# Kernel optimization log

Hardware: AMD Instinct MI355X
Metric: run time of the kernel (lower is better)

The kernel has to match this reference:

```python
import jax, jax.numpy as jnp
import numpy as np

T, B, I, H = 4096, 2048, 1, 10


def setup_inputs() -> dict:
    key = jax.random.key(0)
    ks = jax.random.split(key, 8)
    k = 1.0 / np.sqrt(H)  # torch default init bound for RNN and Linear(10,1)
    u = lambda kk, shape: jax.random.uniform(kk, shape, jnp.float32, -k, k)
    return {
        "x": jax.random.normal(ks[0], (T, B, I), jnp.float32),
        "h": jnp.zeros((1, B, H), jnp.float32),
        "W_ih": u(ks[1], (H, I)),
        "b_ih": u(ks[2], (H,)),
        "W_hh": u(ks[3], (H, H)),
        "b_hh": u(ks[4], (H,)),
        "W_out": u(ks[5], (1, H)),
        "b_out": u(ks[6], (1,)),
    }


def reference(x, h, W_ih, b_ih, W_hh, b_hh, W_out, b_out):
    # Vanilla RNN: h_t = tanh(x_t @ W_ih^T + b_ih + h_{t-1} @ W_hh^T + b_hh)
    b = b_ih + b_hh  # fuse the two biases once

    def step(h_prev, x_t):  # h_prev: [B,H], x_t: [B,I]
        h_new = jnp.tanh(x_t @ W_ih.T + h_prev @ W_hh.T + b)
        return h_new, h_new

    h_last, ys = jax.lax.scan(step, h[0], x)  # ys: [T,B,H]
    out = ys @ W_out.T + b_out  # [T,B,1]
    return out, h_last[None]  # h: [1,B,H]
```

## Files before the change

### kernel.cpp

```cpp
#include <hip/hip_runtime.h>

#define T_STEPS 4096
#define BATCH   2048
#define HID     10
#define UB      16

__device__ __forceinline__ void issue16(float (&xr)[UB], const float* base) {
#pragma unroll
    for (int u = 0; u < UB; ++u)
        asm volatile("global_load_dword %0, %1, off"
                     : "=v"(xr[u]) : "v"(base + (size_t)u * BATCH) : "memory");
}
#define BIND16(a) "+v"(a[0]),"+v"(a[1]),"+v"(a[2]),"+v"(a[3]),"+v"(a[4]), \
    "+v"(a[5]),"+v"(a[6]),"+v"(a[7]),"+v"(a[8]),"+v"(a[9]),"+v"(a[10]),   \
    "+v"(a[11]),"+v"(a[12]),"+v"(a[13]),"+v"(a[14]),"+v"(a[15])
__device__ __forceinline__ void wait1_bind(float (&xr)[UB]) {
    asm volatile("s_waitcnt vmcnt(1)" : BIND16(xr) :: "memory");
}
__device__ __forceinline__ void wait0_bind(float (&xr)[UB]) {
    asm volatile("s_waitcnt vmcnt(0)" : BIND16(xr) :: "memory");
}

#define STEP_HEAD \
    "v_fma_f32 %[c0], %[wih2], %[x], %[bj2]\n\t"                                    \
    "v_fmac_f32 %[c0], %[r], %[w0]\n\t"                                             \
    "v_mul_f32_dpp %[c1], %[r], %[w1] row_ror:1 row_mask:0xf bank_mask:0xf\n\t"     \
    "v_fmac_f32_dpp %[c0], %[r], %[w2] row_ror:2 row_mask:0xf bank_mask:0xf\n\t"    \
    "v_fmac_f32_dpp %[c1], %[r], %[w3] row_ror:3 row_mask:0xf bank_mask:0xf\n\t"    \
    "v_fmac_f32_dpp %[c0], %[r], %[w4] row_ror:4 row_mask:0xf bank_mask:0xf\n\t"    \
    "v_fmac_f32_dpp %[c1], %[r], %[w5] row_ror:5 row_mask:0xf bank_mask:0xf\n\t"    \
    "v_fmac_f32_dpp %[c0], %[r], %[w6] row_ror:6 row_mask:0xf bank_mask:0xf\n\t"    \
    "v_fmac_f32_dpp %[c1], %[r], %[w7] row_ror:7 row_mask:0xf bank_mask:0xf\n\t"    \
    "v_fmac_f32_dpp %[c0], %[r], %[w8] row_ror:8 row_mask:0xf bank_mask:0xf\n\t"    \
    "v_fmac_f32_dpp %[c1], %[r], %[w9] row_ror:9 row_mask:0xf bank_mask:0xf\n\t"    \
    "v_fmac_f32_dpp %[c0], %[r], %[w10] row_ror:10 row_mask:0xf bank_mask:0xf\n\t"  \
    "v_fmac_f32_dpp %[c1], %[r], %[w11] row_ror:11 row_mask:0xf bank_mask:0xf\n\t"  \
    "v_fmac_f32_dpp %[c0], %[r], %[w12] row_ror:12 row_mask:0xf bank_mask:0xf\n\t"  \
    "v_fmac_f32_dpp %[c1], %[r], %[w13] row_ror:13 row_mask:0xf bank_mask:0xf\n\t"  \
    "v_fmac_f32_dpp %[c0], %[r], %[w14] row_ror:14 row_mask:0xf bank_mask:0xf\n\t"  \
    "v_fmac_f32_dpp %[c1], %[r], %[w15] row_ror:15 row_mask:0xf bank_mask:0xf\n\t"  \
    "v_add_f32 %[c0], %[c0], %[c1]\n\t"                                             \
    "v_exp_f32 %[ex], %[c0]\n\t"                                                    \
    "s_nop 0\n\t"                                                                   \
    "v_add_f32 %[ex], 1.0, %[ex]\n\t"

#define STEP_TAIL \
    "v_rcp_f32 %[r], %[ex]\n\t"                                                     \
    "s_nop 0"

#define PKDPP(N) "v_fmac_f32_dpp %[pk], %[c0], %[m] row_ror:" #N " row_mask:0xf bank_mask:0xf\n\t"
#define PKPLAIN  "v_fmac_f32 %[pk], %[c0], %[m]\n\t"

#define DEF_STEP(SUF, PKLINE_) \
__device__ __forceinline__ void step_##SUF(float& r, float& pk, float x, \
        float wih2, float bj2, float m, const float (&w)[16]) { \
    float c0, c1, ex; \
    asm volatile( STEP_HEAD PKLINE_ STEP_TAIL \
        : [c0]"=&v"(c0), [c1]"=&v"(c1), [ex]"=&v"(ex), \
          [r]"+v"(r), [pk]"+v"(pk) \
        : [x]"v"(x), [wih2]"v"(wih2), [bj2]"v"(bj2), [m]"v"(m), \
          [w0]"v"(w[0]),  [w1]"v"(w[1]),  [w2]"v"(w[2]),  [w3]"v"(w[3]), \
          [w4]"v"(w[4]),  [w5]"v"(w[5]),  [w6]"v"(w[6]),  [w7]"v"(w[7]), \
          [w8]"v"(w[8]),  [w9]"v"(w[9]),  [w10]"v"(w[10]),[w11]"v"(w[11]), \
          [w12]"v"(w[12]),[w13]"v"(w[13]),[w14]"v"(w[14]),[w15]"v"(w[15])); \
}

DEF_STEP(r0,  PKPLAIN)
DEF_STEP(r1,  PKDPP(1))
DEF_STEP(r2,  PKDPP(2))
DEF_STEP(r3,  PKDPP(3))
DEF_STEP(r4,  PKDPP(4))
DEF_STEP(r5,  PKDPP(5))
DEF_STEP(r6,  PKDPP(6))
DEF_STEP(r7,  PKDPP(7))
DEF_STEP(r8,  PKDPP(8))
DEF_STEP(r9,  PKDPP(9))
DEF_STEP(r10, PKDPP(10))
DEF_STEP(r11, PKDPP(11))
DEF_STEP(r12, PKDPP(12))
DEF_STEP(r13, PKDPP(13))
DEF_STEP(r14, PKDPP(14))
DEF_STEP(r15, PKDPP(15))

template<int U>
__device__ __forceinline__ void step_u(float& r, float& pk, float x,
                                       float wih2, float bj2,
                                       const float (&km)[16],
                                       const float (&w)[16]) {
    constexpr int ROT = (U + 5) & 15;
    const float m = km[(U + 15) & 15];
    if constexpr (ROT == 0)       step_r0 (r, pk, x, wih2, bj2, m, w);
    else if constexpr (ROT == 1)  step_r1 (r, pk, x, wih2, bj2, m, w);
    else if constexpr (ROT == 2)  step_r2 (r, pk, x, wih2, bj2, m, w);
    else if constexpr (ROT == 3)  step_r3 (r, pk, x, wih2, bj2, m, w);
    else if constexpr (ROT == 4)  step_r4 (r, pk, x, wih2, bj2, m, w);
    else if constexpr (ROT == 5)  step_r5 (r, pk, x, wih2, bj2, m, w);
    else if constexpr (ROT == 6)  step_r6 (r, pk, x, wih2, bj2, m, w);
    else if constexpr (ROT == 7)  step_r7 (r, pk, x, wih2, bj2, m, w);
    else if constexpr (ROT == 8)  step_r8 (r, pk, x, wih2, bj2, m, w);
    else if constexpr (ROT == 9)  step_r9 (r, pk, x, wih2, bj2, m, w);
    else if constexpr (ROT == 10) step_r10(r, pk, x, wih2, bj2, m, w);
    else if constexpr (ROT == 11) step_r11(r, pk, x, wih2, bj2, m, w);
    else if constexpr (ROT == 12) step_r12(r, pk, x, wih2, bj2, m, w);
    else if constexpr (ROT == 13) step_r13(r, pk, x, wih2, bj2, m, w);
    else if constexpr (ROT == 14) step_r14(r, pk, x, wih2, bj2, m, w);
    else                          step_r15(r, pk, x, wih2, bj2, m, w);
}

template<int U>
__device__ __forceinline__ void run16(float& r, float& pk, const float (&xr)[UB],
                                      float wih2, float bj2,
                                      const float (&km)[16],
                                      const float (&w)[16]) {
    if constexpr (U < UB) {
        step_u<U>(r, pk, xr[U], wih2, bj2, km, w);
        run16<U + 1>(r, pk, xr, wih2, bj2, km, w);
    }
}

__device__ __forceinline__ void finish_reduce(float r, float& p, float& pk,
                                              float wo2, float m0) {
    asm volatile(
        "v_mul_f32 %[p], %[wo2], %[r]\n\t"
        "s_nop 1\n\t"
        "v_add_f32_dpp %[p], %[p], %[p] row_ror:8 row_mask:0xf bank_mask:0xf\n\t"
        "s_nop 1\n\t"
        "v_add_f32_dpp %[p], %[p], %[p] row_ror:4 row_mask:0xf bank_mask:0xf\n\t"
        "s_nop 1\n\t"
        "v_add_f32_dpp %[p], %[p], %[p] row_ror:2 row_mask:0xf bank_mask:0xf\n\t"
        "s_nop 1\n\t"
        "v_add_f32_dpp %[p], %[p], %[p] row_ror:1 row_mask:0xf bank_mask:0xf\n\t"
        "s_nop 1\n\t"
        "v_fmac_f32 %[pk], %[p], %[m]"
        : [p]"+v"(p), [pk]"+v"(pk)
        : [r]"v"(r), [wo2]"v"(wo2), [m]"v"(m0));
}

__global__ __launch_bounds__(64, 1) void rnn_kernel(
    const float* __restrict__ x,
    const float* __restrict__ h0,
    const float* __restrict__ W_ih,
    const float* __restrict__ b_ih,
    const float* __restrict__ W_hh,
    const float* __restrict__ b_hh,
    const float* __restrict__ W_out,
    const float* __restrict__ b_out,
    float* __restrict__ out)
{
    const int tid = threadIdx.x;
    const int j   = tid & 15;
    const int b   = (blockIdx.x << 2) + (tid >> 4);
    const bool jv = (j < HID);
    const int jc  = jv ? j : 0;

    const float CC = 2.88539008177792681472f;

    const float wih = jv ? W_ih[jc] : 0.0f;
    const float bj  = jv ? (b_ih[jc] + b_hh[jc]) : 0.0f;
    const float wo  = jv ? W_out[jc] : 0.0f;

    float wsh[16];
    float wsum = 0.0f;
#pragma unroll
    for (int N = 0; N < 16; ++N) {
        const int k = (j - N) & 15;
        wsh[N] = (jv && k < HID) ? W_hh[jc * HID + k] : 0.0f;
        wsum += wsh[N];
    }

    const float wih2 = CC * wih;
    const float bj2  = CC * (bj + wsum);
    float w2[16];
#pragma unroll
    for (int N = 0; N < 16; ++N) {
        if (jv) {
            w2[N] = -2.0f * CC * wsh[N];
        } else if (j == 10) {
            const int k = (10 - N) & 15;
            w2[N] = (k < HID) ? (-2.0f * W_out[k]) : 0.0f;
        } else {
            w2[N] = 0.0f;
        }
    }
    const float wo2 = -2.0f * wo;
    float c0sum = b_out[0];
#pragma unroll
    for (int k = 0; k < HID; ++k) c0sum += W_out[k];

    float km[16];
#pragma unroll
    for (int i = 0; i < 16; ++i) km[i] = (j == i) ? 1.0f : 0.0f;

    float rval = fmaf(-0.5f, jv ? h0[b * HID + jc] : 0.0f, 0.5f);
    float pk = 0.0f;

    const float* xb = x + b;
    float xA[UB], xB[UB];

    issue16(xA, xb);
    wait0_bind(xA);

    for (int t0 = 0; t0 < T_STEPS; t0 += 2 * UB) {
        wait1_bind(xA);
        issue16(xB, xb + (size_t)(t0 + UB) * BATCH);
        run16<0>(rval, pk, xA, wih2, bj2, km, w2);
        {
            const int tj = t0 + ((j == 15) ? -1 : j);
            if (tj >= 0) out[(size_t)tj * BATCH + b] = pk + c0sum;
        }
        pk = 0.0f;

        wait1_bind(xB);
        const float* xsrc = (t0 + 2 * UB < T_STEPS)
                          ? (xb + (size_t)(t0 + 2 * UB) * BATCH) : xb;
        issue16(xA, xsrc);
        run16<0>(rval, pk, xB, wih2, bj2, km, w2);
        {
            const int t1 = t0 + UB;
            const int tj = t1 + ((j == 15) ? -1 : j);
            out[(size_t)tj * BATCH + b] = pk + c0sum;
        }
        pk = 0.0f;
    }

    wait0_bind(xA);

    float p = 0.0f, pk2 = 0.0f;
    finish_reduce(rval, p, pk2, wo2, km[0]);
    if (j == 0) out[(size_t)(T_STEPS - 1) * BATCH + b] = pk2 + c0sum;

    if (jv) out[(size_t)T_STEPS * BATCH + (size_t)b * HID + j]
                = fmaf(-2.0f, rval, 1.0f);
}

extern "C" void kernel_launch(void* const* d_in, const int* in_sizes, int n_in,
                              void* d_out, int out_size, void* d_ws, size_t ws_size,
                              hipStream_t stream) {
    const float* x     = (const float*)d_in[0];
    const float* h0    = (const float*)d_in[1];
    const float* W_ih  = (const float*)d_in[2];
    const float* b_ih  = (const float*)d_in[3];
    const float* W_hh  = (const float*)d_in[4];
    const float* b_hh  = (const float*)d_in[5];
    const float* W_out = (const float*)d_in[6];
    const float* b_out = (const float*)d_in[7];

    rnn_kernel<<<BATCH / 4, 64, 0, stream>>>(
        x, h0, W_ih, b_ih, W_hh, b_hh, W_out, b_out, (float*)d_out);
}
```

Measured before the change: 324.5 us.

## Split each batch's recurrent matvec across wave halves using permlane32 swap

```diff
diff --git a/kernel.cpp b/kernel.cpp
--- a/kernel.cpp
+++ b/kernel.cpp
@@ -22,47 +22,44 @@
 }
 
 #define STEP_HEAD \
-    "v_fma_f32 %[c0], %[wih2], %[x], %[bj2]\n\t"                                    \
-    "v_fmac_f32 %[c0], %[r], %[w0]\n\t"                                             \
-    "v_mul_f32_dpp %[c1], %[r], %[w1] row_ror:1 row_mask:0xf bank_mask:0xf\n\t"     \
-    "v_fmac_f32_dpp %[c0], %[r], %[w2] row_ror:2 row_mask:0xf bank_mask:0xf\n\t"    \
-    "v_fmac_f32_dpp %[c1], %[r], %[w3] row_ror:3 row_mask:0xf bank_mask:0xf\n\t"    \
-    "v_fmac_f32_dpp %[c0], %[r], %[w4] row_ror:4 row_mask:0xf bank_mask:0xf\n\t"    \
-    "v_fmac_f32_dpp %[c1], %[r], %[w5] row_ror:5 row_mask:0xf bank_mask:0xf\n\t"    \
-    "v_fmac_f32_dpp %[c0], %[r], %[w6] row_ror:6 row_mask:0xf bank_mask:0xf\n\t"    \
-    "v_fmac_f32_dpp %[c1], %[r], %[w7] row_ror:7 row_mask:0xf bank_mask:0xf\n\t"    \
-    "v_fmac_f32_dpp %[c0], %[r], %[w8] row_ror:8 row_mask:0xf bank_mask:0xf\n\t"    \
-    "v_fmac_f32_dpp %[c1], %[r], %[w9] row_ror:9 row_mask:0xf bank_mask:0xf\n\t"    \
-    "v_fmac_f32_dpp %[c0], %[r], %[w10] row_ror:10 row_mask:0xf bank_mask:0xf\n\t"  \
-    "v_fmac_f32_dpp %[c1], %[r], %[w11] row_ror:11 row_mask:0xf bank_mask:0xf\n\t"  \
-    "v_fmac_f32_dpp %[c0], %[r], %[w12] row_ror:12 row_mask:0xf bank_mask:0xf\n\t"  \
-    "v_fmac_f32_dpp %[c1], %[r], %[w13] row_ror:13 row_mask:0xf bank_mask:0xf\n\t"  \
-    "v_fmac_f32_dpp %[c0], %[r], %[w14] row_ror:14 row_mask:0xf bank_mask:0xf\n\t"  \
-    "v_fmac_f32_dpp %[c1], %[r], %[w15] row_ror:15 row_mask:0xf bank_mask:0xf\n\t"  \
-    "v_add_f32 %[c0], %[c0], %[c1]\n\t"                                             \
-    "v_exp_f32 %[ex], %[c0]\n\t"                                                    \
-    "s_nop 0\n\t"                                                                   \
-    "v_add_f32 %[ex], 1.0, %[ex]\n\t"
+    "v_fma_f32 %[P], %[wih2], %[x], %[bj2]\n\t"                                    \
+    "v_fmac_f32 %[P], %[r], %[w0]\n\t"                                             \
+    "v_fmac_f32_dpp %[P], %[r], %[w1] row_ror:1 row_mask:0xf bank_mask:0xf\n\t"    \
+    "v_fmac_f32_dpp %[P], %[r], %[w2] row_ror:2 row_mask:0xf bank_mask:0xf\n\t"    \
+    "v_fmac_f32_dpp %[P], %[r], %[w3] row_ror:3 row_mask:0xf bank_mask:0xf\n\t"    \
+    "v_fmac_f32_dpp %[P], %[r], %[w4] row_ror:4 row_mask:0xf bank_mask:0xf\n\t"    \
+    "v_fmac_f32_dpp %[P], %[r], %[w5] row_ror:5 row_mask:0xf bank_mask:0xf\n\t"    \
+    "v_fmac_f32_dpp %[P], %[r], %[w6] row_ror:6 row_mask:0xf bank_mask:0xf\n\t"    \
+    "v_fmac_f32_dpp %[P], %[r], %[w7] row_ror:7 row_mask:0xf bank_mask:0xf\n\t"    \
+    "v_mov_b32 %[t], %[P]\n\t"                                                     \
+    "s_nop 0\n\t"                                                                  \
+    "v_permlane32_swap_b32 %[P], %[t]\n\t"                                         \
+    "s_nop 0\n\t"                                                                  \
+    "v_add_f32 %[c], %[P], %[t]\n\t"                                               \
+    "v_exp_f32 %[ex], %[c]\n\t"                                                    \
+    "s_nop 0\n\t"
 
 #define STEP_TAIL \
-    "v_rcp_f32 %[r], %[ex]\n\t"                                                     \
+    "v_add_f32 %[ex], 1.0, %[ex]\n\t"                                              \
+    "s_nop 1\n\t"                                                                  \
+    "v_mov_b32_dpp %[ex], %[ex] row_ror:8 row_mask:0xc bank_mask:0xf\n\t"          \
+    "s_nop 0\n\t"                                                                  \
+    "v_rcp_f32 %[r], %[ex]\n\t"                                                    \
     "s_nop 0"
 
-#define PKDPP(N) "v_fmac_f32_dpp %[pk], %[c0], %[m] row_ror:" #N " row_mask:0xf bank_mask:0xf\n\t"
-#define PKPLAIN  "v_fmac_f32 %[pk], %[c0], %[m]\n\t"
+#define PKDPP(N) "v_fmac_f32_dpp %[pk], %[c], %[m] row_ror:" #N " row_mask:0xf bank_mask:0xf\n\t"
+#define PKPLAIN  "v_fmac_f32 %[pk], %[c], %[m]\n\t"
 
 #define DEF_STEP(SUF, PKLINE_) \
 __device__ __forceinline__ void step_##SUF(float& r, float& pk, float x, \
-        float wih2, float bj2, float m, const float (&w)[16]) { \
-    float c0, c1, ex; \
+        float wih2, float bj2, float m, const float (&w)[8]) { \
+    float P, t, c, ex; \
     asm volatile( STEP_HEAD PKLINE_ STEP_TAIL \
-        : [c0]"=&v"(c0), [c1]"=&v"(c1), [ex]"=&v"(ex), \
+        : [P]"=&v"(P), [t]"=&v"(t), [c]"=&v"(c), [ex]"=&v"(ex), \
           [r]"+v"(r), [pk]"+v"(pk) \
         : [x]"v"(x), [wih2]"v"(wih2), [bj2]"v"(bj2), [m]"v"(m), \
-          [w0]"v"(w[0]),  [w1]"v"(w[1]),  [w2]"v"(w[2]),  [w3]"v"(w[3]), \
-          [w4]"v"(w[4]),  [w5]"v"(w[5]),  [w6]"v"(w[6]),  [w7]"v"(w[7]), \
-          [w8]"v"(w[8]),  [w9]"v"(w[9]),  [w10]"v"(w[10]),[w11]"v"(w[11]), \
-          [w12]"v"(w[12]),[w13]"v"(w[13]),[w14]"v"(w[14]),[w15]"v"(w[15])); \
+          [w0]"v"(w[0]), [w1]"v"(w[1]), [w2]"v"(w[2]), [w3]"v"(w[3]), \
+          [w4]"v"(w[4]), [w5]"v"(w[5]), [w6]"v"(w[6]), [w7]"v"(w[7])); \
 }
 
 DEF_STEP(r0,  PKPLAIN)
@@ -86,7 +83,7 @@
 __device__ __forceinline__ void step_u(float& r, float& pk, float x,
                                        float wih2, float bj2,
                                        const float (&km)[16],
-                                       const float (&w)[16]) {
+                                       const float (&w)[8]) {
     constexpr int ROT = (U + 5) & 15;
     const float m = km[(U + 15) & 15];
     if constexpr (ROT == 0)       step_r0 (r, pk, x, wih2, bj2, m, w);
@@ -111,7 +108,7 @@
 __device__ __forceinline__ void run16(float& r, float& pk, const float (&xr)[UB],
                                       float wih2, float bj2,
                                       const float (&km)[16],
-                                      const float (&w)[16]) {
+                                      const float (&w)[8]) {
     if constexpr (U < UB) {
         step_u<U>(r, pk, xr[U], wih2, bj2, km, w);
         run16<U + 1>(r, pk, xr, wih2, bj2, km, w);
@@ -147,51 +144,42 @@
     const float* __restrict__ b_out,
     float* __restrict__ out)
 {
-    const int tid = threadIdx.x;
-    const int j   = tid & 15;
-    const int b   = (blockIdx.x << 2) + (tid >> 4);
-    const bool jv = (j < HID);
-    const int jc  = jv ? j : 0;
+    const int tid  = threadIdx.x;
+    const int j    = tid & 15;
+    const int bsel = (tid >> 4) & 1;
+    const int half = tid >> 5;
+    const int b    = (blockIdx.x << 1) + bsel;
+    const bool evh = (half == 0);
 
     const float CC = 2.88539008177792681472f;
 
-    const float wih = jv ? W_ih[jc] : 0.0f;
-    const float bj  = jv ? (b_ih[jc] + b_hh[jc]) : 0.0f;
-    const float wo  = jv ? W_out[jc] : 0.0f;
-
-    float wsh[16];
+    float w[8];
+#pragma unroll
+    for (int N = 0; N < 8; ++N) {
+        const int k = (j + 8 * half - N) & 15;
+        float val = 0.0f;
+        if (j < HID && k < HID)        val = -2.0f * CC * W_hh[j * HID + k];
+        else if (j == 10 && k < HID)   val = -2.0f * W_out[k];
+        w[N] = val;
+    }
     float wsum = 0.0f;
-#pragma unroll
-    for (int N = 0; N < 16; ++N) {
-        const int k = (j - N) & 15;
-        wsh[N] = (jv && k < HID) ? W_hh[jc * HID + k] : 0.0f;
-        wsum += wsh[N];
-    }
-
-    const float wih2 = CC * wih;
-    const float bj2  = CC * (bj + wsum);
-    float w2[16];
-#pragma unroll
-    for (int N = 0; N < 16; ++N) {
-        if (jv) {
-            w2[N] = -2.0f * CC * wsh[N];
-        } else if (j == 10) {
-            const int k = (10 - N) & 15;
-            w2[N] = (k < HID) ? (-2.0f * W_out[k]) : 0.0f;
-        } else {
-            w2[N] = 0.0f;
-        }
-    }
-    const float wo2 = -2.0f * wo;
+    if (j < HID) {
+#pragma unroll
+        for (int k = 0; k < HID; ++k) wsum += W_hh[j * HID + k];
+    }
+    const float wih2 = (evh && j < HID) ? CC * W_ih[j] : 0.0f;
+    const float bj2  = (evh && j < HID) ? CC * (b_ih[j] + b_hh[j] + wsum) : 0.0f;
+    const float wo2  = (evh && j < HID) ? (-2.0f * W_out[j]) : 0.0f;
     float c0sum = b_out[0];
 #pragma unroll
     for (int k = 0; k < HID; ++k) c0sum += W_out[k];
 
     float km[16];
 #pragma unroll
-    for (int i = 0; i < 16; ++i) km[i] = (j == i) ? 1.0f : 0.0f;
-
-    float rval = fmaf(-0.5f, jv ? h0[b * HID + jc] : 0.0f, 0.5f);
+    for (int i = 0; i < 16; ++i) km[i] = (evh && j == i) ? 1.0f : 0.0f;
+
+    const int k0 = (j + 8 * half) & 15;
+    float rval = (k0 < HID) ? fmaf(-0.5f, h0[b * HID + k0], 0.5f) : 0.5f;
     float pk = 0.0f;
 
     const float* xb = x + b;
@@ -203,8 +191,8 @@
     for (int t0 = 0; t0 < T_STEPS; t0 += 2 * UB) {
         wait1_bind(xA);
         issue16(xB, xb + (size_t)(t0 + UB) * BATCH);
-        run16<0>(rval, pk, xA, wih2, bj2, km, w2);
-        {
+        run16<0>(rval, pk, xA, wih2, bj2, km, w);
+        if (tid < 32) {
             const int tj = t0 + ((j == 15) ? -1 : j);
             if (tj >= 0) out[(size_t)tj * BATCH + b] = pk + c0sum;
         }
@@ -214,8 +202,8 @@
         const float* xsrc = (t0 + 2 * UB < T_STEPS)
                           ? (xb + (size_t)(t0 + 2 * UB) * BATCH) : xb;
         issue16(xA, xsrc);
-        run16<0>(rval, pk, xB, wih2, bj2, km, w2);
-        {
+        run16<0>(rval, pk, xB, wih2, bj2, km, w);
+        if (tid < 32) {
             const int t1 = t0 + UB;
             const int tj = t1 + ((j == 15) ? -1 : j);
             out[(size_t)tj * BATCH + b] = pk + c0sum;
@@ -227,10 +215,11 @@
 
     float p = 0.0f, pk2 = 0.0f;
     finish_reduce(rval, p, pk2, wo2, km[0]);
-    if (j == 0) out[(size_t)(T_STEPS - 1) * BATCH + b] = pk2 + c0sum;
-
-    if (jv) out[(size_t)T_STEPS * BATCH + (size_t)b * HID + j]
-                = fmaf(-2.0f, rval, 1.0f);
+    if (tid < 32 && j == 0)
+        out[(size_t)(T_STEPS - 1) * BATCH + b] = pk2 + c0sum;
+
+    if (evh && j < HID)
+        out[(size_t)T_STEPS * BATCH + (size_t)b * HID + j] = fmaf(-2.0f, rval, 1.0f);
 }
 
 extern "C" void kernel_launch(void* const* d_in, const int* in_sizes, int n_in,
@@ -245,6 +234,6 @@
     const float* W_out = (const float*)d_in[6];
     const float* b_out = (const float*)d_in[7];
 
-    rnn_kernel<<<BATCH / 4, 64, 0, stream>>>(
+    rnn_kernel<<<BATCH / 2, 64, 0, stream>>>(
         x, h0, W_ih, b_ih, W_hh, b_hh, W_out, b_out, (float*)d_out);
 }
```

Result: no change. 329.2 us (+1.4%).
